# Kernel tuning notes

Measured on AMD Instinct MI355X. Metric: run time of the kernel, lower is better.

## Reference

```python
import jax, jax.numpy as jnp
import numpy as np

A = 200000   # atoms
B = 400000   # directed bonds
H = 300      # hidden_size
AF = 133     # atom_fdim
BF = 147     # bond_fdim
DEPTH = 4    # message passing depth -> DEPTH-1 W_h layers
M = 4096     # molecules in batch


def setup_inputs() -> dict:
    key = jax.random.key(0)
    ks = jax.random.split(key, 10)
    s = 0.05
    f_atoms = jax.random.normal(ks[0], (A, AF), jnp.float32)
    f_bonds = jax.random.normal(ks[1], (B, BF), jnp.float32)
    b_src = jax.random.randint(ks[2], (B,), 0, A, jnp.int32)
    b_dst = jax.random.randint(ks[3], (B,), 0, A, jnp.int32)
    # reverse-bond pairing: bond 2i <-> 2i+1
    b2revb = (jnp.arange(B, dtype=jnp.int32) ^ 1)
    mol_ids = jnp.sort(jax.random.randint(ks[4], (A,), 0, M, jnp.int32))
    W_i_atom = jax.random.normal(ks[5], (AF, H), jnp.float32) * s
    W_i_bond = jax.random.normal(ks[6], (BF, H), jnp.float32) * s
    W_h = jax.random.normal(ks[7], (DEPTH - 1, H, H), jnp.float32) * s
    W_o = jax.random.normal(ks[8], (3 * H, H), jnp.float32) * s
    b_o = jnp.zeros((H,), jnp.float32)
    return dict(f_atoms=f_atoms, f_bonds=f_bonds, W_i_atom=W_i_atom,
                W_i_bond=W_i_bond, W_h=W_h, W_o=W_o, b_o=b_o,
                b_src=b_src, b_dst=b_dst, b2revb=b2revb, mol_ids=mol_ids)


def reference(f_atoms, f_bonds, W_i_atom, W_i_bond, W_h, W_o, b_o,
              b_src, b_dst, b2revb, mol_ids):
    relu = jax.nn.relu
    input_atom = relu(f_atoms @ W_i_atom)   # [A, H]
    input_bond = relu(f_bonds @ W_i_bond)   # [B, H]

    def step(message, Wd):
        # scatter-sum incoming bond messages onto destination atoms
        a_msg = jax.ops.segment_sum(message, b_dst, num_segments=A)  # [A, H]
        # gather back to bonds, subtract reverse-bond message (D-MPNN)
        m = a_msg[b_src] - message[b2revb]                           # [B, H]
        return relu(input_bond + m @ Wd), None

    message, _ = jax.lax.scan(step, input_bond, W_h)  # DEPTH-1 iterations

    a_msg = jax.ops.segment_sum(message, b_dst, num_segments=A)      # [A, H]
    a_input = jnp.concatenate([input_atom, a_msg, input_atom * a_msg], axis=-1)
    atom_h = relu(a_input @ W_o + b_o)                               # [A, H]

    # mean readout per molecule
    sums = jax.ops.segment_sum(atom_h, mol_ids, num_segments=M)      # [M, H]
    counts = jax.ops.segment_sum(jnp.ones((A,), atom_h.dtype), mol_ids, num_segments=M)
    return sums / jnp.clip(counts, 1.0)[:, None]
```

## Files before the change

kernel.cpp:

```cpp
#include <hip/hip_runtime.h>
#include <stdint.h>

#define H   300
#define HP  320
#define CAP 32

using bf8 = __attribute__((ext_vector_type(8))) short;
using f4  = __attribute__((ext_vector_type(4))) float;

__device__ __forceinline__ float bf2f(unsigned short u){
    union { unsigned int i; float f; } v; v.i = ((unsigned int)u) << 16; return v.f;
}
__device__ __forceinline__ unsigned short f2bf(float x){
    unsigned int u = __builtin_bit_cast(unsigned int, x);
    u = (u + 0x7FFFu + ((u >> 16) & 1u)) >> 16;
    return (unsigned short)u;
}

__global__ void fill_k(const int* __restrict__ b_dst, int* __restrict__ cnt,
                       int* __restrict__ bucket, int nB){
    int e = blockIdx.x * 256 + threadIdx.x;
    if (e >= nB) return;
    int d = b_dst[e];
    int slot = atomicAdd(&cnt[d], 1);
    if (slot < CAP) bucket[(long)d * CAP + slot] = e;
}

__global__ void prep_wt(const float* __restrict__ W, unsigned short* __restrict__ Wt,
                        int Kact, int Kp){
    int idx = blockIdx.x * 256 + threadIdx.x;
    if (idx >= 320 * Kp) return;
    int n = idx / Kp, k = idx % Kp;
    float v = (n < H && k < Kact) ? W[(long)k * H + n] : 0.f;
    Wt[idx] = f2bf(v);
}

__global__ void prep_wto(const float* __restrict__ W, unsigned short* __restrict__ Wt){
    int idx = blockIdx.x * 256 + threadIdx.x;
    if (idx >= 320 * 960) return;
    int n = idx / 960, k = idx % 960;
    int blk = k / HP, kk = k % HP;
    float v = (n < H && kk < H) ? W[((long)blk * H + kk) * H + n] : 0.f;
    Wt[idx] = f2bf(v);
}

template<int MODE>
__global__ __launch_bounds__(256, 3)
void gemm_k(const float* __restrict__ Afp, int Kact,
            const unsigned short* __restrict__ Wt,
            const unsigned short* __restrict__ bfA,
            const unsigned short* __restrict__ bfB,
            const float* __restrict__ b_o,
            unsigned short* __restrict__ outb)
{
    constexpr int KS   = (MODE == 0) ? 5 : 10;
    constexpr int SEC  = (MODE == 3) ? 3 : 1;
    constexpr int Ktot = (MODE == 0) ? 160 : (MODE == 3 ? 960 : 320);

    __shared__ char ldsA[64 * 640];

    const int tid = threadIdx.x;
    const int rowBase = blockIdx.x * 64;
    const int r = tid >> 2, c = tid & 3;
    const int e = rowBase + r;

    auto aoff = [&](int row, int uc)->int {
        return row * 640 + ((uc * 2) ^ ((row & 7) << 4));
    };

    auto stageA = [&](int sec){
        #pragma unroll
        for (int i = 0; i < KS; i++){
            const int kk0 = i * 32 + c * 8;
            bf8 v;
            if constexpr (MODE == 0){
                #pragma unroll
                for (int j = 0; j < 8; j++){
                    int k = kk0 + j;
                    float f = (k < Kact) ? Afp[(long)e * Kact + k] : 0.f;
                    v[j] = (short)f2bf(f);
                }
            } else if constexpr (MODE == 4){
                v = *(const bf8*)(bfA + (long)e * HP + kk0);
            } else {
                if (sec == 0){
                    v = *(const bf8*)(bfA + (long)e * HP + kk0);
                } else if (sec == 1){
                    v = *(const bf8*)(bfB + (long)e * HP + kk0);
                } else {
                    bf8 a = *(const bf8*)(bfA + (long)e * HP + kk0);
                    bf8 b = *(const bf8*)(bfB + (long)e * HP + kk0);
                    #pragma unroll
                    for (int q = 0; q < 8; q++)
                        v[q] = (short)f2bf(bf2f((unsigned short)a[q]) * bf2f((unsigned short)b[q]));
                }
            }
            *(bf8*)(ldsA + aoff(r, kk0)) = v;
        }
    };

    const int w    = tid >> 6;
    const int lane = tid & 63;
    const int lr   = lane & 15;
    const int g    = lane >> 4;

    bf8 b0[5], b1[5];
    auto loadB = [&](int t, bf8* dst){
        #pragma unroll
        for (int n = 0; n < 5; n++)
            dst[n] = *(const bf8*)(Wt + (long)(w * 80 + n * 16 + lr) * Ktot + t * 32 + g * 8);
    };

    f4 acc[4][5];
    #pragma unroll
    for (int m = 0; m < 4; m++)
        #pragma unroll
        for (int n = 0; n < 5; n++)
            acc[m][n] = (f4){0.f, 0.f, 0.f, 0.f};

    auto compute = [&](int ks, bf8* bb){
        bf8 af[4];
        #pragma unroll
        for (int m = 0; m < 4; m++)
            af[m] = *(const bf8*)(ldsA + aoff(m * 16 + lr, ks * 32 + g * 8));
        #pragma unroll
        for (int m = 0; m < 4; m++)
            #pragma unroll
            for (int n = 0; n < 5; n++)
                acc[m][n] = __builtin_amdgcn_mfma_f32_16x16x32_bf16(af[m], bb[n], acc[m][n], 0, 0, 0);
    };

    #pragma unroll
    for (int sec = 0; sec < SEC; ++sec){
        if (sec > 0) __syncthreads();
        stageA(sec);
        loadB(sec * KS, b0);
        __syncthreads();
        #pragma unroll
        for (int i = 0; i < KS; i += 2){
            const int t = sec * KS + i;
            if (i + 1 < KS) loadB(t + 1, b1);
            compute(i, b0);
            if (i + 2 < KS) loadB(t + 2, b0);
            if (i + 1 < KS) compute(i + 1, b1);
        }
    }

    const int rgrp = g * 4;
    #pragma unroll
    for (int m = 0; m < 4; m++){
        #pragma unroll
        for (int n = 0; n < 5; n++){
            int col = w * 80 + n * 16 + lr;
            #pragma unroll
            for (int q = 0; q < 4; q++){
                int row = m * 16 + rgrp + q;
                int gr  = rowBase + row;
                float v = acc[m][n][q];
                if constexpr (MODE == 3) v += (col < H ? b_o[col] : 0.f);
                if constexpr (MODE != 4) v = fmaxf(v, 0.f);
                outb[(long)gr * HP + col] = f2bf(v);
            }
        }
    }
}

__global__ __launch_bounds__(256)
void comb_k(const unsigned short* __restrict__ MW,
            const unsigned short* __restrict__ bond_in,
            const int* __restrict__ b_src, const int* __restrict__ b2revb,
            const int* __restrict__ cnt, const int* __restrict__ bucket,
            unsigned short* __restrict__ out, int nB){
    int t = blockIdx.x * 256 + threadIdx.x;
    if (t >= nB * 40) return;
    int e = t / 40, ch = t % 40;
    int k0 = ch * 8;
    int s   = b_src[e];
    int rev = b2revb[e];
    int dg = cnt[s]; if (dg > CAP) dg = CAP;
    long base = (long)s * CAP;
    int be0 = 0, be1 = 0, be2 = 0, be3 = 0;
    if (dg > 0) be0 = bucket[base + 0];
    if (dg > 1) be1 = bucket[base + 1];
    if (dg > 2) be2 = bucket[base + 2];
    if (dg > 3) be3 = bucket[base + 3];
    bf8 bi = *(const bf8*)(bond_in + (long)e * HP + k0);
    bf8 rv = *(const bf8*)(MW + (long)rev * HP + k0);
    bf8 m0, m1, m2, m3;
    if (dg > 0) m0 = *(const bf8*)(MW + (long)be0 * HP + k0);
    if (dg > 1) m1 = *(const bf8*)(MW + (long)be1 * HP + k0);
    if (dg > 2) m2 = *(const bf8*)(MW + (long)be2 * HP + k0);
    if (dg > 3) m3 = *(const bf8*)(MW + (long)be3 * HP + k0);
    float sacc[8];
    #pragma unroll
    for (int q = 0; q < 8; q++)
        sacc[q] = bf2f((unsigned short)bi[q]) - bf2f((unsigned short)rv[q]);
    auto addv = [&](bf8 mm){
        #pragma unroll
        for (int q = 0; q < 8; q++) sacc[q] += bf2f((unsigned short)mm[q]);
    };
    if (dg > 0) addv(m0);
    if (dg > 1) addv(m1);
    if (dg > 2) addv(m2);
    if (dg > 3) addv(m3);
    for (int j = 4; j < dg; ++j){
        int be = bucket[base + j];
        addv(*(const bf8*)(MW + (long)be * HP + k0));
    }
    bf8 v;
    #pragma unroll
    for (int q = 0; q < 8; q++) v[q] = (short)f2bf(fmaxf(sacc[q], 0.f));
    *(bf8*)(out + (long)e * HP + k0) = v;
}

__global__ __launch_bounds__(256)
void amsg_k(const unsigned short* __restrict__ msg, const int* __restrict__ cnt,
            const int* __restrict__ bucket, unsigned short* __restrict__ amsg,
            int nA){
    int t = blockIdx.x * 256 + threadIdx.x;
    if (t >= nA * 40) return;
    int a = t / 40, ch = t % 40;
    int k0 = ch * 8;
    int dg = cnt[a]; if (dg > CAP) dg = CAP;
    long base = (long)a * CAP;
    int be0 = 0, be1 = 0, be2 = 0, be3 = 0;
    if (dg > 0) be0 = bucket[base + 0];
    if (dg > 1) be1 = bucket[base + 1];
    if (dg > 2) be2 = bucket[base + 2];
    if (dg > 3) be3 = bucket[base + 3];
    bf8 m0, m1, m2, m3;
    if (dg > 0) m0 = *(const bf8*)(msg + (long)be0 * HP + k0);
    if (dg > 1) m1 = *(const bf8*)(msg + (long)be1 * HP + k0);
    if (dg > 2) m2 = *(const bf8*)(msg + (long)be2 * HP + k0);
    if (dg > 3) m3 = *(const bf8*)(msg + (long)be3 * HP + k0);
    float s[8];
    #pragma unroll
    for (int q = 0; q < 8; q++) s[q] = 0.f;
    auto addv = [&](bf8 mm){
        #pragma unroll
        for (int q = 0; q < 8; q++) s[q] += bf2f((unsigned short)mm[q]);
    };
    if (dg > 0) addv(m0);
    if (dg > 1) addv(m1);
    if (dg > 2) addv(m2);
    if (dg > 3) addv(m3);
    for (int j = 4; j < dg; ++j)
        addv(*(const bf8*)(msg + (long)bucket[base + j] * HP + k0));
    bf8 v;
    #pragma unroll
    for (int q = 0; q < 8; q++) v[q] = (short)f2bf(s[q]);
    *(bf8*)(amsg + (long)a * HP + k0) = v;
}

__global__ __launch_bounds__(320)
void readout_k(const unsigned short* __restrict__ atom_h,
               const int* __restrict__ mol_ids, int nAtoms,
               float* __restrict__ out){
    int m = blockIdx.x;
    int t = threadIdx.x;
    int lo = 0, hi = nAtoms;
    while (lo < hi){ int mid = (lo + hi) >> 1; if (mol_ids[mid] < m) lo = mid + 1; else hi = mid; }
    int lo2 = lo, hi2 = nAtoms;
    while (lo2 < hi2){ int mid = (lo2 + hi2) >> 1; if (mol_ids[mid] < m + 1) lo2 = mid + 1; else hi2 = mid; }
    if (t < H){
        float s = 0.f;
        for (int a = lo; a < lo2; ++a) s += bf2f(atom_h[(long)a * HP + t]);
        int c2 = lo2 - lo;
        out[(long)m * H + t] = s / (float)(c2 > 0 ? c2 : 1);
    }
}

extern "C" void kernel_launch(void* const* d_in, const int* in_sizes, int n_in,
                              void* d_out, int out_size, void* d_ws, size_t ws_size,
                              hipStream_t stream){
    const float* f_atoms  = (const float*)d_in[0];
    const float* f_bonds  = (const float*)d_in[1];
    const float* W_i_atom = (const float*)d_in[2];
    const float* W_i_bond = (const float*)d_in[3];
    const float* W_h      = (const float*)d_in[4];
    const float* W_o      = (const float*)d_in[5];
    const float* b_o      = (const float*)d_in[6];
    const int* b_src   = (const int*)d_in[7];
    const int* b_dst   = (const int*)d_in[8];
    const int* b2revb  = (const int*)d_in[9];
    const int* mol_ids = (const int*)d_in[10];

    const int nA = in_sizes[10];
    const int nB = in_sizes[7];
    const int nM = out_size / H;

    char* p = (char*)d_ws;
    auto alloc = [&](size_t bytes){ char* q = p; p += (bytes + 255) & ~(size_t)255; return q; };
    unsigned short* Wt_ia = (unsigned short*)alloc((size_t)320 * 160 * 2);
    unsigned short* Wt_ib = (unsigned short*)alloc((size_t)320 * 160 * 2);
    unsigned short* Wt_h  = (unsigned short*)alloc((size_t)3 * 320 * 320 * 2);
    unsigned short* Wt_o  = (unsigned short*)alloc((size_t)320 * 960 * 2);
    int* cnt    = (int*)alloc((size_t)nA * 4);
    int* bucket = (int*)alloc((size_t)nA * CAP * 4);
    unsigned short* input_atom = (unsigned short*)alloc((size_t)nA * HP * 2);
    unsigned short* input_bond = (unsigned short*)alloc((size_t)nB * HP * 2);
    unsigned short* msgA = (unsigned short*)alloc((size_t)nB * HP * 2);
    unsigned short* MW   = (unsigned short*)alloc((size_t)nB * HP * 2);
    unsigned short* amsg   = MW;
    unsigned short* atom_h = input_bond;

    if ((size_t)(p - (char*)d_ws) > ws_size) return;

    hipMemsetAsync(cnt, 0, (size_t)nA * 4, stream);
    fill_k<<<dim3((nB + 255) / 256), dim3(256), 0, stream>>>(b_dst, cnt, bucket, nB);

    prep_wt<<<dim3((320*160 + 255)/256), dim3(256), 0, stream>>>(W_i_atom, Wt_ia, 133, 160);
    prep_wt<<<dim3((320*160 + 255)/256), dim3(256), 0, stream>>>(W_i_bond, Wt_ib, 147, 160);
    for (int d = 0; d < 3; d++)
        prep_wt<<<dim3((320*320 + 255)/256), dim3(256), 0, stream>>>(
            W_h + (size_t)d * H * H, Wt_h + (size_t)d * 320 * 320, 300, 320);
    prep_wto<<<dim3((320*960 + 255)/256), dim3(256), 0, stream>>>(W_o, Wt_o);

    gemm_k<0><<<dim3(nA/64), dim3(256), 0, stream>>>(
        f_atoms, 133, Wt_ia, nullptr, nullptr, nullptr, input_atom);
    gemm_k<0><<<dim3(nB/64), dim3(256), 0, stream>>>(
        f_bonds, 147, Wt_ib, nullptr, nullptr, nullptr, input_bond);

    const int combGrid = (nB * 40 + 255) / 256;
    gemm_k<4><<<dim3(nB/64), dim3(256), 0, stream>>>(
        nullptr, 0, Wt_h + 0 * 320 * 320, input_bond, nullptr, nullptr, MW);
    comb_k<<<dim3(combGrid), dim3(256), 0, stream>>>(
        MW, input_bond, b_src, b2revb, cnt, bucket, msgA, nB);
    gemm_k<4><<<dim3(nB/64), dim3(256), 0, stream>>>(
        nullptr, 0, Wt_h + 1 * 320 * 320, msgA, nullptr, nullptr, MW);
    comb_k<<<dim3(combGrid), dim3(256), 0, stream>>>(
        MW, input_bond, b_src, b2revb, cnt, bucket, msgA, nB);
    gemm_k<4><<<dim3(nB/64), dim3(256), 0, stream>>>(
        nullptr, 0, Wt_h + 2 * 320 * 320, msgA, nullptr, nullptr, MW);
    comb_k<<<dim3(combGrid), dim3(256), 0, stream>>>(
        MW, input_bond, b_src, b2revb, cnt, bucket, msgA, nB);

    amsg_k<<<dim3((nA * 40 + 255) / 256), dim3(256), 0, stream>>>(msgA, cnt, bucket, amsg, nA);

    gemm_k<3><<<dim3(nA/64), dim3(256), 0, stream>>>(
        nullptr, 0, Wt_o, input_atom, amsg, b_o, atom_h);

    readout_k<<<dim3(nM), dim3(320), 0, stream>>>(atom_h, mol_ids, nA, (float*)d_out);
}
```

Measured before the change: 2.322 ms.

## Make GEMMs persistent with double-buffered async LDS loads and precomputed inputs

Replaces the per-tile GEMM with a persistent kernel that walks tiles in a grid-stride loop. The next A tile is streamed into a second LDS buffer with global_load_lds while the current one is computed, and B fragments are prefetched through a three-slot ring. The fp32 inputs are converted to padded bf16 by a separate pass, and the atom_message × input_atom product is computed inside amsg_k, so every GEMM stage is a plain bf16 DMA. This hides global-load latency behind MFMA work, at the cost of extra conversion passes, more LDS per block (fewer resident blocks), and reuse of the MW buffer as scratch.

```diff
diff --git a/kernel.cpp b/kernel.cpp
--- a/kernel.cpp
+++ b/kernel.cpp
@@ -44,123 +44,137 @@
     Wt[idx] = f2bf(v);
 }
 
-template<int MODE>
-__global__ __launch_bounds__(256, 3)
-void gemm_k(const float* __restrict__ Afp, int Kact,
+__global__ __launch_bounds__(256)
+void conv_in(const float* __restrict__ X, int rows, int Kact,
+             unsigned short* __restrict__ Y){
+    int t = blockIdx.x * 256 + threadIdx.x;
+    if (t >= rows * 20) return;
+    int row = t / 20, k0 = (t % 20) * 8;
+    bf8 v;
+    #pragma unroll
+    for (int j = 0; j < 8; j++){
+        int k = k0 + j;
+        float f = (k < Kact) ? X[(long)row * Kact + k] : 0.f;
+        v[j] = (short)f2bf(f);
+    }
+    *(bf8*)(Y + (long)row * 160 + k0) = v;
+}
+
+template<int RL, int SEC, int EPI>
+__global__ __launch_bounds__(256, 2)
+void gemm_p(const unsigned short* __restrict__ A0,
+            const unsigned short* __restrict__ A1,
+            const unsigned short* __restrict__ A2,
             const unsigned short* __restrict__ Wt,
-            const unsigned short* __restrict__ bfA,
-            const unsigned short* __restrict__ bfB,
             const float* __restrict__ b_o,
-            unsigned short* __restrict__ outb)
+            unsigned short* __restrict__ outb,
+            int nTiles)
 {
-    constexpr int KS   = (MODE == 0) ? 5 : 10;
-    constexpr int SEC  = (MODE == 3) ? 3 : 1;
-    constexpr int Ktot = (MODE == 0) ? 160 : (MODE == 3 ? 960 : 320);
-
-    __shared__ char ldsA[64 * 640];
-
-    const int tid = threadIdx.x;
-    const int rowBase = blockIdx.x * 64;
-    const int r = tid >> 2, c = tid & 3;
-    const int e = rowBase + r;
-
-    auto aoff = [&](int row, int uc)->int {
-        return row * 640 + ((uc * 2) ^ ((row & 7) << 4));
-    };
-
-    auto stageA = [&](int sec){
-        #pragma unroll
-        for (int i = 0; i < KS; i++){
-            const int kk0 = i * 32 + c * 8;
-            bf8 v;
-            if constexpr (MODE == 0){
-                #pragma unroll
-                for (int j = 0; j < 8; j++){
-                    int k = kk0 + j;
-                    float f = (k < Kact) ? Afp[(long)e * Kact + k] : 0.f;
-                    v[j] = (short)f2bf(f);
-                }
-            } else if constexpr (MODE == 4){
-                v = *(const bf8*)(bfA + (long)e * HP + kk0);
-            } else {
-                if (sec == 0){
-                    v = *(const bf8*)(bfA + (long)e * HP + kk0);
-                } else if (sec == 1){
-                    v = *(const bf8*)(bfB + (long)e * HP + kk0);
-                } else {
-                    bf8 a = *(const bf8*)(bfA + (long)e * HP + kk0);
-                    bf8 b = *(const bf8*)(bfB + (long)e * HP + kk0);
-                    #pragma unroll
-                    for (int q = 0; q < 8; q++)
-                        v[q] = (short)f2bf(bf2f((unsigned short)a[q]) * bf2f((unsigned short)b[q]));
-                }
-            }
-            *(bf8*)(ldsA + aoff(r, kk0)) = v;
-        }
-    };
-
+    constexpr int KS     = RL / 32;
+    constexpr int CHUNKS = RL / 8;
+    constexpr int XM     = (CHUNKS == 40) ? 7 : 3;
+    constexpr int TILEB  = 64 * RL * 2;
+    constexpr int ROUNDS = TILEB / 4096;
+    constexpr int Ktot   = SEC * RL;
+
+    __shared__ char lds[2 * TILEB];
+
+    const int tid  = threadIdx.x;
     const int w    = tid >> 6;
     const int lane = tid & 63;
     const int lr   = lane & 15;
     const int g    = lane >> 4;
 
-    bf8 b0[5], b1[5];
-    auto loadB = [&](int t, bf8* dst){
+    const unsigned short* Ap[3] = {A0, A1, A2};
+
+    auto dma = [&](const unsigned short* src, int rowBase, int buf){
+        const char* gbase = (const char*)(src + (long)rowBase * RL);
+        char* lbase = lds + buf * TILEB + (w * 64) * 16;
+        #pragma unroll
+        for (int rd = 0; rd < ROUNDS; rd++){
+            int f   = rd * 256 + tid;
+            int row = f / CHUNKS;
+            int c   = f - row * CHUNKS;
+            int cs  = c ^ (row & XM);
+            const char* gp = gbase + ((long)row * CHUNKS + cs) * 16;
+            __builtin_amdgcn_global_load_lds(
+                (const __attribute__((address_space(1))) void*)gp,
+                (__attribute__((address_space(3))) void*)(lbase + rd * 4096),
+                16, 0, 0);
+        }
+    };
+
+    auto aoff = [&](int buf, int row, int chunk)->int {
+        return buf * TILEB + row * (RL * 2) + ((chunk ^ (row & XM)) << 4);
+    };
+
+    bf8 bb[3][5];
+    auto loadB = [&](int ks, int slot){
         #pragma unroll
         for (int n = 0; n < 5; n++)
-            dst[n] = *(const bf8*)(Wt + (long)(w * 80 + n * 16 + lr) * Ktot + t * 32 + g * 8);
+            bb[slot][n] = *(const bf8*)(Wt + (long)(w * 80 + n * 16 + lr) * Ktot + ks * 32 + g * 8);
     };
 
     f4 acc[4][5];
-    #pragma unroll
-    for (int m = 0; m < 4; m++)
-        #pragma unroll
-        for (int n = 0; n < 5; n++)
-            acc[m][n] = (f4){0.f, 0.f, 0.f, 0.f};
-
-    auto compute = [&](int ks, bf8* bb){
-        bf8 af[4];
-        #pragma unroll
-        for (int m = 0; m < 4; m++)
-            af[m] = *(const bf8*)(ldsA + aoff(m * 16 + lr, ks * 32 + g * 8));
+
+    int tile = blockIdx.x;
+    if (tile >= nTiles) return;
+    dma(Ap[0], tile * 64, 0);
+    __syncthreads();
+
+    int buf = 0;
+    for (; tile < nTiles; tile += gridDim.x){
         #pragma unroll
         for (int m = 0; m < 4; m++)
             #pragma unroll
             for (int n = 0; n < 5; n++)
-                acc[m][n] = __builtin_amdgcn_mfma_f32_16x16x32_bf16(af[m], bb[n], acc[m][n], 0, 0, 0);
-    };
-
-    #pragma unroll
-    for (int sec = 0; sec < SEC; ++sec){
-        if (sec > 0) __syncthreads();
-        stageA(sec);
-        loadB(sec * KS, b0);
-        __syncthreads();
-        #pragma unroll
-        for (int i = 0; i < KS; i += 2){
-            const int t = sec * KS + i;
-            if (i + 1 < KS) loadB(t + 1, b1);
-            compute(i, b0);
-            if (i + 2 < KS) loadB(t + 2, b0);
-            if (i + 1 < KS) compute(i + 1, b1);
-        }
-    }
-
-    const int rgrp = g * 4;
-    #pragma unroll
-    for (int m = 0; m < 4; m++){
-        #pragma unroll
-        for (int n = 0; n < 5; n++){
-            int col = w * 80 + n * 16 + lr;
+                acc[m][n] = (f4){0.f, 0.f, 0.f, 0.f};
+
+        #pragma unroll
+        for (int sec = 0; sec < SEC; ++sec){
+            {
+                int ns = sec + 1, ntile = tile;
+                if (ns == SEC){ ns = 0; ntile = tile + (int)gridDim.x; }
+                if (ntile < nTiles) dma(Ap[ns], ntile * 64, buf ^ 1);
+            }
+            loadB(sec * KS + 0, 0);
+            loadB(sec * KS + 1, 1);
+            loadB(sec * KS + 2, 2);
+
             #pragma unroll
-            for (int q = 0; q < 4; q++){
-                int row = m * 16 + rgrp + q;
-                int gr  = rowBase + row;
-                float v = acc[m][n][q];
-                if constexpr (MODE == 3) v += (col < H ? b_o[col] : 0.f);
-                if constexpr (MODE != 4) v = fmaxf(v, 0.f);
-                outb[(long)gr * HP + col] = f2bf(v);
+            for (int i = 0; i < KS; i++){
+                bf8 af[4];
+                #pragma unroll
+                for (int m = 0; m < 4; m++)
+                    af[m] = *(const bf8*)(lds + aoff(buf, m * 16 + lr, i * 4 + g));
+                #pragma unroll
+                for (int m = 0; m < 4; m++)
+                    #pragma unroll
+                    for (int n = 0; n < 5; n++)
+                        acc[m][n] = __builtin_amdgcn_mfma_f32_16x16x32_bf16(af[m], bb[i % 3][n], acc[m][n], 0, 0, 0);
+                if (i + 3 < KS) loadB(sec * KS + i + 3, i % 3);
             }
+
+            if (sec == SEC - 1){
+                const int rgrp = g * 4;
+                #pragma unroll
+                for (int m = 0; m < 4; m++){
+                    #pragma unroll
+                    for (int n = 0; n < 5; n++){
+                        int col = w * 80 + n * 16 + lr;
+                        #pragma unroll
+                        for (int q = 0; q < 4; q++){
+                            int gr = tile * 64 + m * 16 + rgrp + q;
+                            float v = acc[m][n][q];
+                            if constexpr (EPI == 2) v += (col < H ? b_o[col] : 0.f);
+                            if constexpr (EPI != 1) v = fmaxf(v, 0.f);
+                            outb[(long)gr * HP + col] = f2bf(v);
+                        }
+                    }
+                }
+            }
+            __syncthreads();
+            buf ^= 1;
         }
     }
 }
@@ -215,7 +229,9 @@
 
 __global__ __launch_bounds__(256)
 void amsg_k(const unsigned short* __restrict__ msg, const int* __restrict__ cnt,
-            const int* __restrict__ bucket, unsigned short* __restrict__ amsg,
+            const int* __restrict__ bucket,
+            const unsigned short* __restrict__ input_atom,
+            unsigned short* __restrict__ amsg, unsigned short* __restrict__ prod,
             int nA){
     int t = blockIdx.x * 256 + threadIdx.x;
     if (t >= nA * 40) return;
@@ -228,6 +244,7 @@
     if (dg > 1) be1 = bucket[base + 1];
     if (dg > 2) be2 = bucket[base + 2];
     if (dg > 3) be3 = bucket[base + 3];
+    bf8 ia = *(const bf8*)(input_atom + (long)a * HP + k0);
     bf8 m0, m1, m2, m3;
     if (dg > 0) m0 = *(const bf8*)(msg + (long)be0 * HP + k0);
     if (dg > 1) m1 = *(const bf8*)(msg + (long)be1 * HP + k0);
@@ -246,10 +263,14 @@
     if (dg > 3) addv(m3);
     for (int j = 4; j < dg; ++j)
         addv(*(const bf8*)(msg + (long)bucket[base + j] * HP + k0));
-    bf8 v;
-    #pragma unroll
-    for (int q = 0; q < 8; q++) v[q] = (short)f2bf(s[q]);
-    *(bf8*)(amsg + (long)a * HP + k0) = v;
+    bf8 va, vp;
+    #pragma unroll
+    for (int q = 0; q < 8; q++){
+        va[q] = (short)f2bf(s[q]);
+        vp[q] = (short)f2bf(s[q] * bf2f((unsigned short)ia[q]));
+    }
+    *(bf8*)(amsg + (long)a * HP + k0) = va;
+    *(bf8*)(prod + (long)a * HP + k0) = vp;
 }
 
 __global__ __launch_bounds__(320)
@@ -301,7 +322,10 @@
     unsigned short* input_bond = (unsigned short*)alloc((size_t)nB * HP * 2);
     unsigned short* msgA = (unsigned short*)alloc((size_t)nB * HP * 2);
     unsigned short* MW   = (unsigned short*)alloc((size_t)nB * HP * 2);
+    unsigned short* fa_bf  = MW;
+    unsigned short* fb_bf  = MW + (size_t)nA * 160;
     unsigned short* amsg   = MW;
+    unsigned short* prod   = MW + (size_t)nA * HP;
     unsigned short* atom_h = input_bond;
 
     if ((size_t)(p - (char*)d_ws) > ws_size) return;
@@ -315,30 +339,31 @@
         prep_wt<<<dim3((320*320 + 255)/256), dim3(256), 0, stream>>>(
             W_h + (size_t)d * H * H, Wt_h + (size_t)d * 320 * 320, 300, 320);
     prep_wto<<<dim3((320*960 + 255)/256), dim3(256), 0, stream>>>(W_o, Wt_o);
-
-    gemm_k<0><<<dim3(nA/64), dim3(256), 0, stream>>>(
-        f_atoms, 133, Wt_ia, nullptr, nullptr, nullptr, input_atom);
-    gemm_k<0><<<dim3(nB/64), dim3(256), 0, stream>>>(
-        f_bonds, 147, Wt_ib, nullptr, nullptr, nullptr, input_bond);
+    conv_in<<<dim3((nA*20 + 255)/256), dim3(256), 0, stream>>>(f_atoms, nA, 133, fa_bf);
+    conv_in<<<dim3((nB*20 + 255)/256), dim3(256), 0, stream>>>(f_bonds, nB, 147, fb_bf);
+
+    const int tilesA = nA / 64, tilesB = nB / 64;
+
+    gemm_p<160,1,0><<<dim3(1024), dim3(256), 0, stream>>>(
+        fa_bf, nullptr, nullptr, Wt_ia, nullptr, input_atom, tilesA);
+    gemm_p<160,1,0><<<dim3(1024), dim3(256), 0, stream>>>(
+        fb_bf, nullptr, nullptr, Wt_ib, nullptr, input_bond, tilesB);
 
     const int combGrid = (nB * 40 + 255) / 256;
-    gemm_k<4><<<dim3(nB/64), dim3(256), 0, stream>>>(
-        nullptr, 0, Wt_h + 0 * 320 * 320, input_bond, nullptr, nullptr, MW);
-    comb_k<<<dim3(combGrid), dim3(256), 0, stream>>>(
-        MW, input_bond, b_src, b2revb, cnt, bucket, msgA, nB);
-    gemm_k<4><<<dim3(nB/64), dim3(256), 0, stream>>>(
-        nullptr, 0, Wt_h + 1 * 320 * 320, msgA, nullptr, nullptr, MW);
-    comb_k<<<dim3(combGrid), dim3(256), 0, stream>>>(
-        MW, input_bond, b_src, b2revb, cnt, bucket, msgA, nB);
-    gemm_k<4><<<dim3(nB/64), dim3(256), 0, stream>>>(
-        nullptr, 0, Wt_h + 2 * 320 * 320, msgA, nullptr, nullptr, MW);
-    comb_k<<<dim3(combGrid), dim3(256), 0, stream>>>(
-        MW, input_bond, b_src, b2revb, cnt, bucket, msgA, nB);
-
-    amsg_k<<<dim3((nA * 40 + 255) / 256), dim3(256), 0, stream>>>(msgA, cnt, bucket, amsg, nA);
-
-    gemm_k<3><<<dim3(nA/64), dim3(256), 0, stream>>>(
-        nullptr, 0, Wt_o, input_atom, amsg, b_o, atom_h);
+    const unsigned short* msg_cur = input_bond;
+    for (int d = 0; d < 3; d++){
+        gemm_p<320,1,1><<<dim3(512), dim3(256), 0, stream>>>(
+            msg_cur, nullptr, nullptr, Wt_h + (size_t)d * 320 * 320, nullptr, MW, tilesB);
+        comb_k<<<dim3(combGrid), dim3(256), 0, stream>>>(
+            MW, input_bond, b_src, b2revb, cnt, bucket, msgA, nB);
+        msg_cur = msgA;
+    }
+
+    amsg_k<<<dim3((nA * 40 + 255) / 256), dim3(256), 0, stream>>>(
+        msgA, cnt, bucket, input_atom, amsg, prod, nA);
+
+    gemm_p<320,3,2><<<dim3(512), dim3(256), 0, stream>>>(
+        input_atom, amsg, prod, Wt_o, b_o, atom_h, tilesA);
 
     readout_k<<<dim3(nM), dim3(320), 0, stream>>>(atom_h, mol_ids, nA, (float*)d_out);
 }
```

New measurement: 2.556 ms. +10.1%, slower.
